# Kernel optimization log

Measured on AMD Instinct MI355X. Metric: run time of the kernel, lower is better.

The kernel has to match this reference:

```python
import jax, jax.numpy as jnp
import numpy as np

FILTER = 3
STRIDE = 1


def setup_inputs() -> dict:
    key = jax.random.key(0)
    ks = jax.random.split(key, 6)
    B, P, N, d_in, d_ein, d_model = 16, 4, 4096, 128, 32, 128
    e_dim = FILTER * (FILTER - 1) * d_ein  # 192
    adj = jax.random.uniform(ks[0], (N, N), jnp.float32)
    features = jax.random.normal(ks[1], (B, N, d_in), jnp.float32)
    edge_features = jax.random.normal(ks[2], (B, N, e_dim), jnp.float32)
    mask = jax.random.uniform(ks[3], (P, N, 1), jnp.float32)
    W = jax.random.normal(ks[4], (FILTER * d_in + e_dim, d_model), jnp.float32) * 0.02
    b = jnp.zeros((d_model,), jnp.float32)
    return dict(adj=adj, features=features, edge_features=edge_features, mask=mask, W=W, b=b)


def reference(adj, features, edge_features, mask, W, b):
    Fs, S = FILTER, STRIDE
    B, N, d_in = features.shape
    # padding rule from _padding(): below_pad = filter - (N % stride or stride)
    below_pad = N % S
    below_pad = S if below_pad == 0 else below_pad
    below_pad = Fs - below_pad  # = 2 for stride=1, filter=3
    n_out = (N + below_pad - Fs) // S + 1  # = N

    feat_pad = jnp.pad(features, ((0, 0), (0, below_pad), (0, 0)))
    idx = jnp.arange(n_out)[:, None] * S + jnp.arange(Fs)[None, :]  # [n_out, F]
    win = feat_pad[:, idx, :]  # [B, n_out, F, d_in] (gather = torch unfold windows)
    jump = win.mean(axis=2)    # features.unfold(...).sum(-1)/filter -> [B, n_out, d_in]
    # torch unfold puts filter dim last: [B, n_out, d_in, F]; flatten(-2,-1) is d_in-major
    feat_flat = jnp.swapaxes(win, -1, -2).reshape(B, n_out, Fs * d_in)

    mask_pad = jnp.pad(mask, ((0, 0), (0, below_pad), (0, 0)))
    m = mask_pad[:, idx, :].max(axis=2)  # [P, n_out, 1]

    feat_cat = jnp.concatenate([feat_flat, edge_features], axis=-1)  # [B, n_out, 576]
    out = jax.nn.relu(feat_cat @ W + b)  # dropout is identity in eval
    res = out + jump  # residual (res=True)

    P = m.shape[0]
    d_model = out.shape[-1]
    out_m = (m * out.reshape(-1, P, n_out, d_model)).reshape(-1, n_out, d_model)
    res_m = (m * res.reshape(-1, P, n_out, d_model)).reshape(-1, n_out, d_model)
    return adj, res_m, out_m, m
```

## Files before the change

kernel.cpp:

```cpp
#include <hip/hip_runtime.h>
#include <hip/hip_bf16.h>

typedef __attribute__((ext_vector_type(8))) short short8;
typedef __attribute__((ext_vector_type(4))) float floatx4;

#define NN     4096
#define DIN    128
#define EDIM   192
#define DMODEL 128

__device__ __forceinline__ unsigned short f2bf(float f) {
    union { float f; unsigned int i; } x; x.f = f;
    unsigned int u = x.i;
    u += 0x7FFFu + ((u >> 16) & 1u);
    return (unsigned short)(u >> 16);
}

__device__ __forceinline__ unsigned int pk2(float lo, float hi) {
    union { __hip_bfloat162 v; unsigned int u; } cv;
    cv.v = __float22bfloat162_rn(make_float2(lo, hi));
    return cv.u;
}

__device__ __forceinline__ short8 cvt8(const float4 a, const float4 b) {
    union { short8 s; unsigned int u[4]; } r;
    r.u[0] = pk2(a.x, a.y);
    r.u[1] = pk2(a.z, a.w);
    r.u[2] = pk2(b.x, b.y);
    r.u[3] = pk2(b.z, b.w);
    return r.s;
}

__global__ void prep_w(const float* __restrict__ W, unsigned short* __restrict__ wf) {
    const int t = blockIdx.x * 256 + threadIdx.x;
    const int jj   = t & 7;
    const int lane = (t >> 3) & 63;
    const int ct   = (t >> 9) & 7;
    const int gs   = t >> 12;
    const int kt = gs * 32 + ((lane >> 4) << 3) + jj;
    const int korig = (kt < 384) ? ((kt & 127) * 3 + (kt >> 7)) : kt;
    const int n = ct * 16 + (lane & 15);
    wf[t] = f2bf(W[korig * DMODEL + n]);
}

__global__ __launch_bounds__(256, 2) void main_k(
    const float* __restrict__ feat,
    const float* __restrict__ edgef,
    const unsigned short* __restrict__ wfrag,
    const float* __restrict__ bias,
    const float* __restrict__ mask,
    const floatx4* __restrict__ adj4,
    floatx4* __restrict__ o_adj4,
    float* __restrict__ o_res,
    float* __restrict__ o_out,
    float* __restrict__ o_m)
{
    __shared__ float m3s[128];

    const int tid  = threadIdx.x;
    const int lane = tid & 63;
    const int wv   = tid >> 6;
    const int nn   = lane & 15;
    const int quad = lane >> 4;

    const int blk = blockIdx.x;
    const int b   = blk >> 5;
    const int i0  = (blk & 31) << 7;
    const int p   = b & 3;

    const float* fb = feat  + (size_t)b * NN * DIN;
    const float* eb = edgef + (size_t)b * NN * EDIM;
    const int rowb = i0 + wv * 32 + nn;
    const int adjbase = blk * 256 + tid;

    if (tid < 128) {
        const int i = i0 + tid;
        float v = mask[p * NN + i];
        if (i + 1 < NN) v = fmaxf(v, mask[p * NN + i + 1]);
        if (i + 2 < NN) v = fmaxf(v, mask[p * NN + i + 2]);
        m3s[tid] = v;
        if (b < 4) o_m[p * NN + i] = v;
    }
    __syncthreads();

    const short8* wf8 = (const short8*)wfrag;
    const float4 zf4 = make_float4(0.f, 0.f, 0.f, 0.f);

    float4  Ar[2][4];
    short8  Br[2][8];
    floatx4 Ja[2], Jb[2];

    auto loadB = [&](int s, short8* B) {
        #pragma unroll
        for (int ct = 0; ct < 8; ++ct)
            B[ct] = wf8[(s * 8 + ct) * 64 + lane];
    };

    auto loadA = [&](int s, float4* A) {
        if (s < 12) {
            const int j = s >> 2, sl = s & 3;
            const int off = sl * 32 + quad * 8;
            const int r0 = rowb + j;
            A[0] = zf4; A[1] = zf4;
            if (r0 < NN) {
                const float* sp = fb + (size_t)r0 * DIN + off;
                A[0] = *(const float4*)sp; A[1] = *(const float4*)(sp + 4);
            }
            const int r1 = rowb + 16 + j;
            A[2] = zf4; A[3] = zf4;
            if (r1 < NN) {
                const float* sp = fb + (size_t)r1 * DIN + off;
                A[2] = *(const float4*)sp; A[3] = *(const float4*)(sp + 4);
            }
        } else {
            const int eg = s - 12;
            const int off = eg * 32 + quad * 8;
            const float* sp0 = eb + (size_t)rowb * EDIM + off;
            A[0] = *(const float4*)sp0; A[1] = *(const float4*)(sp0 + 4);
            const float* sp1 = eb + (size_t)(rowb + 16) * EDIM + off;
            A[2] = *(const float4*)sp1; A[3] = *(const float4*)(sp1 + 4);
        }
    };

    floatx4 acc[2][8];
    #pragma unroll
    for (int rt = 0; rt < 2; ++rt)
        #pragma unroll
        for (int ct = 0; ct < 8; ++ct)
            acc[rt][ct] = (floatx4){0.f, 0.f, 0.f, 0.f};

    loadB(0, Br[0]);
    loadB(1, Br[1]);
    loadA(0, Ar[0]);
    loadA(1, Ar[1]);
    Ja[0] = __builtin_nontemporal_load(&adj4[adjbase]);
    Jb[0] = __builtin_nontemporal_load(&adj4[adjbase + (size_t)1 * 131072]);
    Ja[1] = __builtin_nontemporal_load(&adj4[adjbase + (size_t)2 * 131072]);
    Jb[1] = __builtin_nontemporal_load(&adj4[adjbase + (size_t)3 * 131072]);

    #pragma unroll
    for (int s = 0; s < 18; ++s) {
        const int pr = s & 1;

        const short8 af0 = cvt8(Ar[pr][0], Ar[pr][1]);
        const short8 af1 = cvt8(Ar[pr][2], Ar[pr][3]);

        if (s <= 15) {
            __builtin_nontemporal_store(Ja[pr], &o_adj4[adjbase + (size_t)(2 * s) * 131072]);
            __builtin_nontemporal_store(Jb[pr], &o_adj4[adjbase + (size_t)(2 * s + 1) * 131072]);
        }
        if (s <= 13) {
            Ja[pr] = __builtin_nontemporal_load(&adj4[adjbase + (size_t)(2 * s + 4) * 131072]);
            Jb[pr] = __builtin_nontemporal_load(&adj4[adjbase + (size_t)(2 * s + 5) * 131072]);
        }

        short8 bt[8];
        #pragma unroll
        for (int ct = 0; ct < 8; ++ct)
            bt[ct] = Br[pr][ct];
        if (s <= 15) {
            loadB(s + 2, Br[pr]);
            loadA(s + 2, Ar[pr]);
        }

        #pragma unroll
        for (int ct = 0; ct < 8; ++ct) {
            acc[0][ct] = __builtin_amdgcn_mfma_f32_16x16x32_bf16(af0, bt[ct], acc[0][ct], 0, 0, 0);
            acc[1][ct] = __builtin_amdgcn_mfma_f32_16x16x32_bf16(af1, bt[ct], acc[1][ct], 0, 0, 0);
        }
    }

    float biasv[8];
    #pragma unroll
    for (int ct = 0; ct < 8; ++ct)
        biasv[ct] = bias[ct * 16 + nn];

    const float inv3 = 1.0f / 3.0f;

    #pragma unroll
    for (int rt = 0; rt < 2; ++rt) {
        const int rbase = wv * 32 + rt * 16 + quad * 4;
        float mv[4];
        #pragma unroll
        for (int reg = 0; reg < 4; ++reg)
            mv[reg] = m3s[rbase + reg];
        #pragma unroll
        for (int ct = 0; ct < 8; ++ct) {
            const int col = ct * 16 + nn;
            float fv[6];
            #pragma unroll
            for (int t6 = 0; t6 < 6; ++t6) {
                const int row = i0 + rbase + t6;
                fv[t6] = (row < NN) ? fb[(size_t)row * DIN + col] : 0.f;
            }
            #pragma unroll
            for (int reg = 0; reg < 4; ++reg) {
                float o = acc[rt][ct][reg] + biasv[ct];
                o = fmaxf(o, 0.f);
                const float jmp = (fv[reg] + fv[reg + 1] + fv[reg + 2]) * inv3;
                const size_t off = ((size_t)b * NN + (i0 + rbase + reg)) * DMODEL + col;
                const float mm = mv[reg];
                __builtin_nontemporal_store(mm * o, &o_out[off]);
                __builtin_nontemporal_store(mm * (o + jmp), &o_res[off]);
            }
        }
    }
}

extern "C" void kernel_launch(void* const* d_in, const int* in_sizes, int n_in,
                              void* d_out, int out_size, void* d_ws, size_t ws_size,
                              hipStream_t stream) {
    const float* adj   = (const float*)d_in[0];
    const float* feat  = (const float*)d_in[1];
    const float* edgef = (const float*)d_in[2];
    const float* mask  = (const float*)d_in[3];
    const float* W     = (const float*)d_in[4];
    const float* bias  = (const float*)d_in[5];

    float* out   = (float*)d_out;
    float* o_adj = out;
    float* o_res = out + (size_t)16777216;
    float* o_out = o_res + (size_t)8388608;
    float* o_m   = o_out + (size_t)8388608;

    unsigned short* wfrag = (unsigned short*)d_ws;

    prep_w<<<288, 256, 0, stream>>>(W, wfrag);
    main_k<<<512, 256, 0, stream>>>(feat, edgef, wfrag, bias, mask,
                                    (const floatx4*)adj, (floatx4*)o_adj,
                                    o_res, o_out, o_m);
}
```

Before: 285.8 us.

## Stage weight fragments via async global-to-LDS loads with a 4-deep ring

Weight fragments move from per-wave register loads into a four-slot shared-memory ring, filled with global_load_lds so each wave loads a quarter of each stage and the block shares it. Hand-written vmcnt waits and barriers order the stages, and schedule barriers fix the instruction order. This is meant to cut redundant global loads and register pressure, and to deepen prefetch. It adds a block-wide barrier every stage and relies on exact vmcnt counts for correctness. The feature-row boundary checks also become clamped loads with selects, so the loads no longer sit behind branches.

```diff
diff --git a/kernel.cpp b/kernel.cpp
--- a/kernel.cpp
+++ b/kernel.cpp
@@ -29,6 +29,13 @@
     r.u[2] = pk2(b.x, b.y);
     r.u[3] = pk2(b.z, b.w);
     return r.s;
+}
+
+__device__ __forceinline__ void gl_lds16(const void* g, void* l) {
+    __builtin_amdgcn_global_load_lds(
+        (const __attribute__((address_space(1))) unsigned int*)g,
+        (__attribute__((address_space(3))) unsigned int*)l,
+        16, 0, 0);
 }
 
 __global__ void prep_w(const float* __restrict__ W, unsigned short* __restrict__ wf) {
@@ -55,6 +62,7 @@
     float* __restrict__ o_out,
     float* __restrict__ o_m)
 {
+    __shared__ __align__(16) char lbuf[4][8192];
     __shared__ float m3s[128];
 
     const int tid  = threadIdx.x;
@@ -81,37 +89,30 @@
         m3s[tid] = v;
         if (b < 4) o_m[p * NN + i] = v;
     }
-    __syncthreads();
-
-    const short8* wf8 = (const short8*)wfrag;
+
+    const char* wsrc = (const char*)wfrag;
     const float4 zf4 = make_float4(0.f, 0.f, 0.f, 0.f);
 
-    float4  Ar[2][4];
-    short8  Br[2][8];
-    floatx4 Ja[2], Jb[2];
-
-    auto loadB = [&](int s, short8* B) {
-        #pragma unroll
-        for (int ct = 0; ct < 8; ++ct)
-            B[ct] = wf8[(s * 8 + ct) * 64 + lane];
+    auto stageB = [&](int s) {
+        const char* src = wsrc + s * 8192 + wv * 2048 + lane * 16;
+        char* dst = &lbuf[s & 3][wv * 2048];
+        gl_lds16(src, dst);
+        gl_lds16(src + 1024, dst + 1024);
     };
 
     auto loadA = [&](int s, float4* A) {
         if (s < 12) {
             const int j = s >> 2, sl = s & 3;
             const int off = sl * 32 + quad * 8;
-            const int r0 = rowb + j;
-            A[0] = zf4; A[1] = zf4;
-            if (r0 < NN) {
-                const float* sp = fb + (size_t)r0 * DIN + off;
-                A[0] = *(const float4*)sp; A[1] = *(const float4*)(sp + 4);
-            }
+            const float* sp0 = fb + (size_t)(rowb + j) * DIN + off;
+            A[0] = *(const float4*)sp0; A[1] = *(const float4*)(sp0 + 4);
             const int r1 = rowb + 16 + j;
-            A[2] = zf4; A[3] = zf4;
-            if (r1 < NN) {
-                const float* sp = fb + (size_t)r1 * DIN + off;
-                A[2] = *(const float4*)sp; A[3] = *(const float4*)(sp + 4);
-            }
+            const int r1c = (r1 < NN) ? r1 : (NN - 1);
+            const float* sp1 = fb + (size_t)r1c * DIN + off;
+            const float4 v0 = *(const float4*)sp1;
+            const float4 v1 = *(const float4*)(sp1 + 4);
+            A[2] = (r1 < NN) ? v0 : zf4;
+            A[3] = (r1 < NN) ? v1 : zf4;
         } else {
             const int eg = s - 12;
             const int off = eg * 32 + quad * 8;
@@ -129,46 +130,71 @@
         for (int ct = 0; ct < 8; ++ct)
             acc[rt][ct] = (floatx4){0.f, 0.f, 0.f, 0.f};
 
-    loadB(0, Br[0]);
-    loadB(1, Br[1]);
-    loadA(0, Ar[0]);
-    loadA(1, Ar[1]);
+    float4  Ar[2][4];
+    floatx4 Ja[2], Jb[2];
+
     Ja[0] = __builtin_nontemporal_load(&adj4[adjbase]);
     Jb[0] = __builtin_nontemporal_load(&adj4[adjbase + (size_t)1 * 131072]);
     Ja[1] = __builtin_nontemporal_load(&adj4[adjbase + (size_t)2 * 131072]);
     Jb[1] = __builtin_nontemporal_load(&adj4[adjbase + (size_t)3 * 131072]);
-
-    #pragma unroll
-    for (int s = 0; s < 18; ++s) {
-        const int pr = s & 1;
-
-        const short8 af0 = cvt8(Ar[pr][0], Ar[pr][1]);
-        const short8 af1 = cvt8(Ar[pr][2], Ar[pr][3]);
-
-        if (s <= 15) {
-            __builtin_nontemporal_store(Ja[pr], &o_adj4[adjbase + (size_t)(2 * s) * 131072]);
-            __builtin_nontemporal_store(Jb[pr], &o_adj4[adjbase + (size_t)(2 * s + 1) * 131072]);
-        }
-        if (s <= 13) {
-            Ja[pr] = __builtin_nontemporal_load(&adj4[adjbase + (size_t)(2 * s + 4) * 131072]);
-            Jb[pr] = __builtin_nontemporal_load(&adj4[adjbase + (size_t)(2 * s + 5) * 131072]);
-        }
-
-        short8 bt[8];
-        #pragma unroll
-        for (int ct = 0; ct < 8; ++ct)
-            bt[ct] = Br[pr][ct];
-        if (s <= 15) {
-            loadB(s + 2, Br[pr]);
-            loadA(s + 2, Ar[pr]);
-        }
-
-        #pragma unroll
-        for (int ct = 0; ct < 8; ++ct) {
-            acc[0][ct] = __builtin_amdgcn_mfma_f32_16x16x32_bf16(af0, bt[ct], acc[0][ct], 0, 0, 0);
-            acc[1][ct] = __builtin_amdgcn_mfma_f32_16x16x32_bf16(af1, bt[ct], acc[1][ct], 0, 0, 0);
-        }
+    loadA(0, Ar[0]);
+    __builtin_amdgcn_sched_barrier(0);
+    stageB(0); stageB(1); stageB(2);
+    asm volatile("s_waitcnt vmcnt(4) lgkmcnt(0)" ::: "memory");
+    __builtin_amdgcn_s_barrier();
+
+#define STAGE(S, NW)                                                                         \
+    {                                                                                        \
+        constexpr int s = (S);                                                               \
+        constexpr int pr = s & 1;                                                            \
+        if (s <= 15) {                                                                       \
+            __builtin_nontemporal_store(Ja[pr], &o_adj4[adjbase + (size_t)(2 * s) * 131072]);     \
+            __builtin_nontemporal_store(Jb[pr], &o_adj4[adjbase + (size_t)(2 * s + 1) * 131072]); \
+        }                                                                                    \
+        if (s <= 13) {                                                                       \
+            Ja[pr] = __builtin_nontemporal_load(&adj4[adjbase + (size_t)(2 * s + 4) * 131072]);   \
+            Jb[pr] = __builtin_nontemporal_load(&adj4[adjbase + (size_t)(2 * s + 5) * 131072]);   \
+        }                                                                                    \
+        if (s <= 16) loadA(s + 1, Ar[(s + 1) & 1]);                                          \
+        __builtin_amdgcn_sched_barrier(0);                                                   \
+        if (s <= 14) stageB(s + 3);                                                          \
+        __builtin_amdgcn_sched_barrier(0);                                                   \
+        {                                                                                    \
+            const short8* bl = (const short8*)(&lbuf[s & 3][0]);                             \
+            const short8 af0 = cvt8(Ar[pr][0], Ar[pr][1]);                                   \
+            const short8 af1 = cvt8(Ar[pr][2], Ar[pr][3]);                                   \
+            _Pragma("unroll")                                                                \
+            for (int ct = 0; ct < 8; ++ct) {                                                 \
+                const short8 bfr = bl[ct * 64 + lane];                                       \
+                acc[0][ct] = __builtin_amdgcn_mfma_f32_16x16x32_bf16(af0, bfr, acc[0][ct], 0, 0, 0); \
+                acc[1][ct] = __builtin_amdgcn_mfma_f32_16x16x32_bf16(af1, bfr, acc[1][ct], 0, 0, 0); \
+            }                                                                                \
+        }                                                                                    \
+        if (s < 17) {                                                                        \
+            asm volatile("s_waitcnt vmcnt(" #NW ")" ::: "memory");                           \
+            __builtin_amdgcn_s_barrier();                                                    \
+        }                                                                                    \
     }
+
+    STAGE(0, 12)
+    STAGE(1, 20)
+    STAGE(2, 20)
+    STAGE(3, 20)
+    STAGE(4, 20)
+    STAGE(5, 20)
+    STAGE(6, 20)
+    STAGE(7, 20)
+    STAGE(8, 20)
+    STAGE(9, 20)
+    STAGE(10, 20)
+    STAGE(11, 20)
+    STAGE(12, 20)
+    STAGE(13, 20)
+    STAGE(14, 18)
+    STAGE(15, 14)
+    STAGE(16, 10)
+    STAGE(17, 0)
+#undef STAGE
 
     float biasv[8];
     #pragma unroll
```

Result: faster. 267.1 us (-6.5%).
